# Kernel tuning notes

Measured on AMD Instinct MI355X. Metric: run time of the kernel, lower is better.

The kernel has to match this reference:

```python
import jax, jax.numpy as jnp
import numpy as np

LSTM_DIMS = 1024
T = 4096
D = 1024  # per-direction input width; must equal LSTM_DIMS (see original w shape)
CELL_CLIP = 3.0   # tf.raw_ops.BlockLSTM default
FORGET_BIAS = 1.0  # tf.raw_ops.BlockLSTM default


def setup_inputs() -> dict:
    key = jax.random.key(0)
    k1, k2, k3 = jax.random.split(key, 3)
    res_for_1 = jax.random.normal(k1, (1, T, D), dtype=jnp.float32)
    res_back_1 = jax.random.normal(k2, (1, T, D), dtype=jnp.float32)
    # GlorotUniform for w: shape [D + 2*H, 4*H]
    fan_in, fan_out = D + 2 * LSTM_DIMS, 4 * LSTM_DIMS
    limit = np.sqrt(6.0 / (fan_in + fan_out)).astype(np.float32)
    w = jax.random.uniform(k3, (fan_in, fan_out), dtype=jnp.float32,
                           minval=-limit, maxval=limit)
    return {"res_for_1": res_for_1, "res_back_1": res_back_1, "w": w}


def _bilstm(res_for_1, res_back_1, w):
    H = w.shape[1] // 4
    x_dim = 2 * res_for_1.shape[-1]
    # concatenate_lstm: vec[i] = concat(for[i], back[T-1-i]) -> [T, 2D]
    vec_for = jnp.concatenate([res_for_1[0], res_back_1[0][::-1]], axis=-1)
    vec_back = vec_for[::-1]
    xs = jnp.stack([vec_for, vec_back])            # [2, T, 2D]
    w_x, w_h = w[:x_dim], w[x_dim:]                # [2D,4H], [H,4H]
    # precompute input projection as one big GEMM (bias is zeros)
    zx = jnp.einsum('dtf,fg->dtg', xs, w_x)        # [2, T, 4H]

    def step(carry, zx_t):
        c, h = carry
        z = zx_t + h @ w_h                         # [4H]
        zi, zc, zf, zo = jnp.split(z, 4)           # BlockLSTM icfo order
        i = jax.nn.sigmoid(zi)
        ci = jnp.tanh(zc)
        f = jax.nn.sigmoid(zf + FORGET_BIAS)
        cs = jnp.clip(f * c + i * ci, -CELL_CLIP, CELL_CLIP)
        o = jax.nn.sigmoid(zo)
        h = o * jnp.tanh(cs)
        return (cs, h), h

    init = (jnp.zeros((H,), zx.dtype), jnp.zeros((H,), zx.dtype))

    def run(zx_dir):
        _, hs = jax.lax.scan(step, init, zx_dir)
        return hs                                  # [T, H]

    hs = jax.vmap(run)(zx)                         # [2, T, H]
    return hs[0], hs[1]                            # res_for_2, res_back_2


def reference(res_for_1, res_back_1, w):
    return _bilstm(res_for_1, res_back_1, w)
```

## Files before the change

kernel.cpp:

```cpp
#include <hip/hip_runtime.h>

#define T_STEPS 4096
#define HDIM 1024

typedef __bf16 bf16x8 __attribute__((ext_vector_type(8)));
typedef float f32x4 __attribute__((ext_vector_type(4)));
typedef _Float16 half2_t __attribute__((ext_vector_type(2)));

__device__ __forceinline__ unsigned short f2bf(float x) {
  unsigned u = __builtin_bit_cast(unsigned, x);
  u += 0x7fffu + ((u >> 16) & 1u);
  return (unsigned short)(u >> 16);
}
__device__ __forceinline__ float bf2f(unsigned short b) {
  unsigned u = ((unsigned)b) << 16;
  return __builtin_bit_cast(float, u);
}

__global__ __launch_bounds__(256) void build_xs(
    const float* __restrict__ rf, const float* __restrict__ rb,
    unsigned short* __restrict__ xs) {
  int idx = blockIdx.x * 256 + threadIdx.x;
  int e = idx * 4;
  int f = e & 2047;
  int td = e >> 11;
  int t = td & 4095;
  int d = td >> 12;
  bool lower = f < 1024;
  int f2 = f & 1023;
  int trow;
  if (d == 0) trow = lower ? t : (4095 - t);
  else        trow = lower ? (4095 - t) : t;
  const float* src = (lower ? rf : rb) + trow * 1024 + f2;
  float4 v = *(const float4*)src;
  ushort4 o = make_ushort4(f2bf(v.x), f2bf(v.y), f2bf(v.z), f2bf(v.w));
  *(ushort4*)(xs + e) = o;
}

__global__ __launch_bounds__(256) void transpose_wx(
    const float* __restrict__ w, unsigned short* __restrict__ wxT) {
  __shared__ float tile[64][65];
  int bid = blockIdx.x;
  int bf_ = bid / 64;
  int bg = bid % 64;
  int f0 = bf_ * 64, g0 = bg * 64;
  int tid = threadIdx.x;
#pragma unroll
  for (int s = 0; s < 16; ++s) {
    int idx = s * 256 + tid;
    int fl = idx >> 6, gl = idx & 63;
    tile[fl][gl] = w[(size_t)(f0 + fl) * 4096 + g0 + gl];
  }
  __syncthreads();
#pragma unroll
  for (int s = 0; s < 16; ++s) {
    int idx = s * 256 + tid;
    int gl = idx >> 6, fl = idx & 63;
    wxT[(size_t)(g0 + gl) * 2048 + f0 + fl] = f2bf(tile[fl][gl]);
  }
}

__global__ __launch_bounds__(256) void gemm_zx(
    const unsigned short* __restrict__ xs, const unsigned short* __restrict__ wxT,
    unsigned short* __restrict__ zxo) {
  __shared__ uint4 lds[1024];
  char* ldsb = (char*)lds;
  int bid = blockIdx.x;
  int by = bid >> 5;
  int bx = bid & 31;
  int tid = threadIdx.x, lane = tid & 63, wid = tid >> 6;
  int wr = wid >> 1, wc = wid & 1;
  const int arow0 = by * 128, bcol0 = bx * 128;

  f32x4 acc[4][4] = {};

  for (int kt = 0; kt < 64; ++kt) {
    int k0 = kt * 32;
#pragma unroll
    for (int s = 0; s < 2; ++s) {
      int c = tid + 256 * s;
      int L = c * 16;
      int P = L ^ (((L >> 6) & 7) << 4);
      int row = c >> 2, ko = (c & 3) * 8;
      uint4 av = *(const uint4*)(xs  + (size_t)(arow0 + row) * 2048 + k0 + ko);
      uint4 bv = *(const uint4*)(wxT + (size_t)(bcol0 + row) * 2048 + k0 + ko);
      *(uint4*)(ldsb + P) = av;
      *(uint4*)(ldsb + 8192 + P) = bv;
    }
    __syncthreads();

    bf16x8 afr[4], bfr[4];
#pragma unroll
    for (int i = 0; i < 4; ++i) {
      int arow = wr * 64 + i * 16 + (lane & 15);
      int L = arow * 64 + (lane >> 4) * 16;
      int P = L ^ ((arow & 7) << 4);
      afr[i] = *(bf16x8*)(ldsb + P);
      int brow = wc * 64 + i * 16 + (lane & 15);
      int L2 = brow * 64 + (lane >> 4) * 16;
      int P2 = L2 ^ ((brow & 7) << 4);
      bfr[i] = *(bf16x8*)(ldsb + 8192 + P2);
    }
#pragma unroll
    for (int mi = 0; mi < 4; ++mi)
#pragma unroll
      for (int ni = 0; ni < 4; ++ni)
        acc[mi][ni] = __builtin_amdgcn_mfma_f32_16x16x32_bf16(
            afr[mi], bfr[ni], acc[mi][ni], 0, 0, 0);
    __syncthreads();
  }

#pragma unroll
  for (int mi = 0; mi < 4; ++mi)
#pragma unroll
    for (int ni = 0; ni < 4; ++ni)
#pragma unroll
      for (int r = 0; r < 4; ++r) {
        int rrow = arow0 + wr * 64 + mi * 16 + (lane >> 4) * 4 + r;
        int col  = bcol0 + wc * 64 + ni * 16 + (lane & 15);
        zxo[(size_t)rrow * 4096 + col] = f2bf(acc[mi][ni][r]);
      }
}

__global__ __launch_bounds__(256) void pack_whp(
    const float* __restrict__ w, unsigned* __restrict__ whp) {
  int idx = blockIdx.x * 256 + threadIdx.x;
  int gc = idx & 4095;
  int k2 = idx >> 12;
  float w0 = w[(size_t)(2048 + 2 * k2) * 4096 + gc];
  float w1 = w[(size_t)(2048 + 2 * k2 + 1) * 4096 + gc];
  unsigned short a = __builtin_bit_cast(unsigned short, (_Float16)w0);
  unsigned short b = __builtin_bit_cast(unsigned short, (_Float16)w1);
  whp[idx] = ((unsigned)b << 16) | (unsigned)a;
}

__global__ __launch_bounds__(256) void clear_hcom(uint4* __restrict__ p) {
  p[(size_t)blockIdx.x * 256 + threadIdx.x] = uint4{0, 0, 0, 0};
}

__device__ __forceinline__ float sigm(float x) {
  return 1.0f / (1.0f + __expf(-x));
}
__device__ __forceinline__ float tanh_fast(float x) {
  float e = __expf(-2.0f * x);
  return (1.0f - e) / (1.0f + e);
}

__global__ __launch_bounds__(1024, 4) void lstm_rec(
    const unsigned short* __restrict__ zx,
    const unsigned* __restrict__ whp,
    unsigned* __restrict__ hcom) {
  __shared__ unsigned short hstg[16][64];
  __shared__ float part[2][16][64];

  int bid = blockIdx.x;
  int dir = bid >> 6;
  int bslot = bid & 63;
  int jbase = bslot << 4;
  int tid = threadIdx.x;
  int wave = tid >> 6;
  int lane = tid & 63;
  int jj = lane & 15, g = lane >> 4;
  int gcol = (g << 10) + jbase + jj;

  unsigned wpk[32];
  {
    const unsigned* wp = whp + (size_t)(wave * 32) * 4096 + gcol;
#pragma unroll
    for (int i = 0; i < 32; ++i) wpk[i] = wp[(size_t)i * 4096];
#pragma unroll
    for (int i = 0; i < 32; ++i)
      asm volatile("v_mov_b32 %0, %0" : "+v"(wpk[i]));
  }

  float c_reg = 0.0f;
  const unsigned short* zrow = zx + (size_t)dir * T_STEPS * 4096;
  unsigned* hcd = hcom + (size_t)dir * T_STEPS * HDIM;
  const unsigned* hp_slice = hcd + wave * 64 + lane;

  for (int t = 0; t < T_STEPS; ++t) {
    float zxv = 0.0f;
    if (wave == 15) zxv = bf2f(zrow[(size_t)t * 4096 + gcol]);

    unsigned short hbits = 0;
    if (t > 0) {
      const unsigned* hp = hp_slice + (size_t)(t - 1) * HDIM;
      unsigned want = (unsigned)t << 16;
      unsigned v;
      do {
        v = __hip_atomic_load(hp, __ATOMIC_RELAXED, __HIP_MEMORY_SCOPE_AGENT);
      } while (v < want);
      hbits = (unsigned short)v;
    }
    hstg[wave][lane] = hbits;
    asm volatile("s_waitcnt lgkmcnt(0)" ::: "memory");

    const uint4* h4p = (const uint4*)(&hstg[wave][0]);
    float ac0 = 0.f, ac1 = 0.f, ac2 = 0.f, ac3 = 0.f;
#pragma unroll
    for (int i = 0; i < 8; ++i) {
      uint4 hv = h4p[i];
      ac0 = __builtin_amdgcn_fdot2(__builtin_bit_cast(half2_t, wpk[4 * i + 0]),
                                   __builtin_bit_cast(half2_t, hv.x), ac0, false);
      ac1 = __builtin_amdgcn_fdot2(__builtin_bit_cast(half2_t, wpk[4 * i + 1]),
                                   __builtin_bit_cast(half2_t, hv.y), ac1, false);
      ac2 = __builtin_amdgcn_fdot2(__builtin_bit_cast(half2_t, wpk[4 * i + 2]),
                                   __builtin_bit_cast(half2_t, hv.z), ac2, false);
      ac3 = __builtin_amdgcn_fdot2(__builtin_bit_cast(half2_t, wpk[4 * i + 3]),
                                   __builtin_bit_cast(half2_t, hv.w), ac3, false);
    }
    float acc = (ac0 + ac1) + (ac2 + ac3);
    if (wave == 15) acc += zxv;
    part[t & 1][wave][lane] = acc;
    __syncthreads();

    if (wave == 0) {
      float z = 0.f;
#pragma unroll
      for (int q = 0; q < 16; ++q) z += part[t & 1][q][lane];
      float gz = (g == 2) ? z + 1.0f : z;
      float nl = (g == 1) ? tanh_fast(z) : sigm(gz);
      float iv = __shfl(nl, jj, 64);
      float cv = __shfl(nl, 16 + jj, 64);
      float fv = __shfl(nl, 32 + jj, 64);
      float ov = __shfl(nl, 48 + jj, 64);
      if (lane < 16) {
        float cs = fmaf(fv, c_reg, iv * cv);
        cs = fminf(3.0f, fmaxf(-3.0f, cs));
        c_reg = cs;
        float h = ov * tanh_fast(cs);
        unsigned short hb = __builtin_bit_cast(unsigned short, (_Float16)h);
        unsigned pk = ((unsigned)(t + 1) << 16) | (unsigned)hb;
        __hip_atomic_store(&hcd[(size_t)t * HDIM + jbase + lane], pk,
                           __ATOMIC_RELAXED, __HIP_MEMORY_SCOPE_AGENT);
      }
    }
  }
}

__global__ __launch_bounds__(256) void unpack_out(
    const unsigned* __restrict__ hcom, float* __restrict__ out) {
  int i = blockIdx.x * 256 + threadIdx.x;
  uint4 v = ((const uint4*)hcom)[i];
  float4 o;
  o.x = (float)__builtin_bit_cast(_Float16, (unsigned short)v.x);
  o.y = (float)__builtin_bit_cast(_Float16, (unsigned short)v.y);
  o.z = (float)__builtin_bit_cast(_Float16, (unsigned short)v.z);
  o.w = (float)__builtin_bit_cast(_Float16, (unsigned short)v.w);
  ((float4*)out)[i] = o;
}

extern "C" void kernel_launch(void* const* d_in, const int* in_sizes, int n_in,
                              void* d_out, int out_size, void* d_ws, size_t ws_size,
                              hipStream_t stream) {
  const float* rf = (const float*)d_in[0];
  const float* rb = (const float*)d_in[1];
  const float* w  = (const float*)d_in[2];
  float* out = (float*)d_out;

  char* ws = (char*)d_ws;
  unsigned short* zx  = (unsigned short*)ws;
  unsigned short* xs  = (unsigned short*)(ws + (64u << 20));
  unsigned*      hcom = (unsigned*)(ws + (64u << 20));
  unsigned short* wxT = (unsigned short*)(ws + (96u << 20));
  unsigned*      whp  = (unsigned*)(ws + (96u << 20));

  build_xs<<<16384, 256, 0, stream>>>(rf, rb, xs);
  transpose_wx<<<2048, 256, 0, stream>>>(w, wxT);
  gemm_zx<<<2048, 256, 0, stream>>>(xs, wxT, zx);
  pack_whp<<<8192, 256, 0, stream>>>(w, whp);
  clear_hcom<<<8192, 256, 0, stream>>>((uint4*)hcom);
  lstm_rec<<<128, 1024, 0, stream>>>(zx, whp, hcom);
  unpack_out<<<8192, 256, 0, stream>>>(hcom, out);
}
```

Measured before the change: 6.348 ms.

## Exchange hidden state through replicated ring mailboxes and prefetch next zx

Blocks no longer publish h through the full T×H history buffer. They now write it into an 8-slot ring mailbox that is replicated 8 ways (indexed by bid&7), so each block polls a nearby replica and the polling traffic, which was aimed at one cache line per step, is spread out. The final history is written separately with plain stores by wave 1. The zx value for the next step is now prefetched right after the spin-wait, and the large clear_hcom kernel is replaced by a small memset of the mailbox. Risks: the ring depth of 8 is only safe if no block gets more than 8 steps ahead of the others, and the wider writer path adds extra stores on every step.

```diff
diff --git a/kernel.cpp b/kernel.cpp
--- a/kernel.cpp
+++ b/kernel.cpp
@@ -134,10 +134,6 @@
   whp[idx] = ((unsigned)b << 16) | (unsigned)a;
 }
 
-__global__ __launch_bounds__(256) void clear_hcom(uint4* __restrict__ p) {
-  p[(size_t)blockIdx.x * 256 + threadIdx.x] = uint4{0, 0, 0, 0};
-}
-
 __device__ __forceinline__ float sigm(float x) {
   return 1.0f / (1.0f + __expf(-x));
 }
@@ -149,7 +145,8 @@
 __global__ __launch_bounds__(1024, 4) void lstm_rec(
     const unsigned short* __restrict__ zx,
     const unsigned* __restrict__ whp,
-    unsigned* __restrict__ hcom) {
+    unsigned* __restrict__ hcom,
+    unsigned* __restrict__ mbox) {
   __shared__ unsigned short hstg[16][64];
   __shared__ float part[2][16][64];
 
@@ -176,15 +173,15 @@
   float c_reg = 0.0f;
   const unsigned short* zrow = zx + (size_t)dir * T_STEPS * 4096;
   unsigned* hcd = hcom + (size_t)dir * T_STEPS * HDIM;
-  const unsigned* hp_slice = hcd + wave * 64 + lane;
+  const unsigned* mb_r = mbox + (((size_t)(bid & 7) * 2 + dir) * 8) * 1024;
+
+  float zx_cur = 0.0f;
+  if (wave == 15) zx_cur = bf2f(zrow[gcol]);
 
   for (int t = 0; t < T_STEPS; ++t) {
-    float zxv = 0.0f;
-    if (wave == 15) zxv = bf2f(zrow[(size_t)t * 4096 + gcol]);
-
     unsigned short hbits = 0;
     if (t > 0) {
-      const unsigned* hp = hp_slice + (size_t)(t - 1) * HDIM;
+      const unsigned* hp = mb_r + (size_t)((t - 1) & 7) * 1024 + wave * 64 + lane;
       unsigned want = (unsigned)t << 16;
       unsigned v;
       do {
@@ -192,6 +189,12 @@
       } while (v < want);
       hbits = (unsigned short)v;
     }
+    asm volatile("" ::: "memory");
+
+    float zx_nxt = 0.0f;
+    if (wave == 15 && t + 1 < T_STEPS)
+      zx_nxt = bf2f(zrow[(size_t)(t + 1) * 4096 + gcol]);
+
     hstg[wave][lane] = hbits;
     asm volatile("s_waitcnt lgkmcnt(0)" ::: "memory");
 
@@ -210,11 +213,12 @@
                                    __builtin_bit_cast(half2_t, hv.w), ac3, false);
     }
     float acc = (ac0 + ac1) + (ac2 + ac3);
-    if (wave == 15) acc += zxv;
+    if (wave == 15) acc += zx_cur;
     part[t & 1][wave][lane] = acc;
+    zx_cur = zx_nxt;
     __syncthreads();
 
-    if (wave == 0) {
+    if (wave <= 1) {
       float z = 0.f;
 #pragma unroll
       for (int q = 0; q < 16; ++q) z += part[t & 1][q][lane];
@@ -224,15 +228,21 @@
       float cv = __shfl(nl, 16 + jj, 64);
       float fv = __shfl(nl, 32 + jj, 64);
       float ov = __shfl(nl, 48 + jj, 64);
-      if (lane < 16) {
-        float cs = fmaf(fv, c_reg, iv * cv);
-        cs = fminf(3.0f, fmaxf(-3.0f, cs));
-        c_reg = cs;
-        float h = ov * tanh_fast(cs);
-        unsigned short hb = __builtin_bit_cast(unsigned short, (_Float16)h);
-        unsigned pk = ((unsigned)(t + 1) << 16) | (unsigned)hb;
-        __hip_atomic_store(&hcd[(size_t)t * HDIM + jbase + lane], pk,
+      float cs = fmaf(fv, c_reg, iv * cv);
+      cs = fminf(3.0f, fmaxf(-3.0f, cs));
+      c_reg = cs;
+      float h = ov * tanh_fast(cs);
+      unsigned short hb = __builtin_bit_cast(unsigned short, (_Float16)h);
+      unsigned pk = ((unsigned)(t + 1) << 16) | (unsigned)hb;
+      if (wave == 0) {
+        int c = lane >> 4;
+        size_t slot = (size_t)(t & 7) * 1024 + jbase + jj;
+        __hip_atomic_store(&mbox[(((size_t)c * 2 + dir) * 8) * 1024 + slot], pk,
                            __ATOMIC_RELAXED, __HIP_MEMORY_SCOPE_AGENT);
+        __hip_atomic_store(&mbox[(((size_t)(c + 4) * 2 + dir) * 8) * 1024 + slot], pk,
+                           __ATOMIC_RELAXED, __HIP_MEMORY_SCOPE_AGENT);
+      } else if (lane < 16) {
+        hcd[(size_t)t * HDIM + jbase + lane] = pk;
       }
     }
   }
@@ -264,12 +274,15 @@
   unsigned*      hcom = (unsigned*)(ws + (64u << 20));
   unsigned short* wxT = (unsigned short*)(ws + (96u << 20));
   unsigned*      whp  = (unsigned*)(ws + (96u << 20));
+  unsigned*      mbox = (unsigned*)(ws + (104u << 20));
+
+  const size_t mbox_bytes = 8ull * 2 * 8 * 1024 * 4;
 
   build_xs<<<16384, 256, 0, stream>>>(rf, rb, xs);
   transpose_wx<<<2048, 256, 0, stream>>>(w, wxT);
   gemm_zx<<<2048, 256, 0, stream>>>(xs, wxT, zx);
   pack_whp<<<8192, 256, 0, stream>>>(w, whp);
-  clear_hcom<<<8192, 256, 0, stream>>>((uint4*)hcom);
-  lstm_rec<<<128, 1024, 0, stream>>>(zx, whp, hcom);
+  hipMemsetAsync(mbox, 0, mbox_bytes, stream);
+  lstm_rec<<<128, 1024, 0, stream>>>(zx, whp, hcom, mbox);
   unpack_out<<<8192, 256, 0, stream>>>(hcom, out);
 }
```

Result: slower. 6.842 ms (+7.8%).

## Halve recurrent blocks, give each block 32 hidden units, prefetch next zx

Applied to the files above, without the earlier changes.

The recurrent kernel now runs 64 blocks, each owning 32 hidden units, instead of 128 blocks owning 16. Each thread holds two sets of packed recurrent weights and produces two gate columns. The gate shuffle is simplified to xor-32 exchanges, and the next step's zx value is loaded ahead of time so that load overlaps the spin-wait. Fewer blocks means fewer participants in the per-step cross-block handshake and less polling traffic. The cost is twice the register weight storage per thread and more dot-product work per block on the critical path.

```diff
diff --git a/kernel.cpp b/kernel.cpp
--- a/kernel.cpp
+++ b/kernel.cpp
@@ -151,26 +151,28 @@
     const unsigned* __restrict__ whp,
     unsigned* __restrict__ hcom) {
   __shared__ unsigned short hstg[16][64];
-  __shared__ float part[2][16][64];
+  __shared__ float part[2][16][128];
 
   int bid = blockIdx.x;
-  int dir = bid >> 6;
-  int bslot = bid & 63;
-  int jbase = bslot << 4;
+  int dir = bid >> 5;
+  int bslot = bid & 31;
+  int jbase = bslot << 5;
   int tid = threadIdx.x;
   int wave = tid >> 6;
   int lane = tid & 63;
-  int jj = lane & 15, g = lane >> 4;
-  int gcol = (g << 10) + jbase + jj;
-
-  unsigned wpk[32];
+  int jj = lane & 31;
+  int g0 = lane >> 5;
+  int gcol0 = (g0 << 10) + jbase + jj;
+  int gcol1 = gcol0 + 2048;
+
+  unsigned wpk0[32], wpk1[32];
   {
-    const unsigned* wp = whp + (size_t)(wave * 32) * 4096 + gcol;
-#pragma unroll
-    for (int i = 0; i < 32; ++i) wpk[i] = wp[(size_t)i * 4096];
-#pragma unroll
-    for (int i = 0; i < 32; ++i)
-      asm volatile("v_mov_b32 %0, %0" : "+v"(wpk[i]));
+    const unsigned* wp = whp + (size_t)(wave * 32) * 4096 + gcol0;
+#pragma unroll
+    for (int i = 0; i < 32; ++i) {
+      wpk0[i] = wp[(size_t)i * 4096];
+      wpk1[i] = wp[(size_t)i * 4096 + 2048];
+    }
   }
 
   float c_reg = 0.0f;
@@ -178,10 +180,13 @@
   unsigned* hcd = hcom + (size_t)dir * T_STEPS * HDIM;
   const unsigned* hp_slice = hcd + wave * 64 + lane;
 
+  float zx0 = 0.0f, zx1 = 0.0f;
+  if (wave == 15) {
+    zx0 = bf2f(zrow[gcol0]);
+    zx1 = bf2f(zrow[gcol1]);
+  }
+
   for (int t = 0; t < T_STEPS; ++t) {
-    float zxv = 0.0f;
-    if (wave == 15) zxv = bf2f(zrow[(size_t)t * 4096 + gcol]);
-
     unsigned short hbits = 0;
     if (t > 0) {
       const unsigned* hp = hp_slice + (size_t)(t - 1) * HDIM;
@@ -192,40 +197,57 @@
       } while (v < want);
       hbits = (unsigned short)v;
     }
+    asm volatile("" ::: "memory");
+
+    float zx0n = 0.0f, zx1n = 0.0f;
+    if (wave == 15 && t + 1 < T_STEPS) {
+      zx0n = bf2f(zrow[(size_t)(t + 1) * 4096 + gcol0]);
+      zx1n = bf2f(zrow[(size_t)(t + 1) * 4096 + gcol1]);
+    }
+
     hstg[wave][lane] = hbits;
     asm volatile("s_waitcnt lgkmcnt(0)" ::: "memory");
 
     const uint4* h4p = (const uint4*)(&hstg[wave][0]);
-    float ac0 = 0.f, ac1 = 0.f, ac2 = 0.f, ac3 = 0.f;
+    float a0 = 0.f, a1 = 0.f, b0 = 0.f, b1 = 0.f;
 #pragma unroll
     for (int i = 0; i < 8; ++i) {
       uint4 hv = h4p[i];
-      ac0 = __builtin_amdgcn_fdot2(__builtin_bit_cast(half2_t, wpk[4 * i + 0]),
-                                   __builtin_bit_cast(half2_t, hv.x), ac0, false);
-      ac1 = __builtin_amdgcn_fdot2(__builtin_bit_cast(half2_t, wpk[4 * i + 1]),
-                                   __builtin_bit_cast(half2_t, hv.y), ac1, false);
-      ac2 = __builtin_amdgcn_fdot2(__builtin_bit_cast(half2_t, wpk[4 * i + 2]),
-                                   __builtin_bit_cast(half2_t, hv.z), ac2, false);
-      ac3 = __builtin_amdgcn_fdot2(__builtin_bit_cast(half2_t, wpk[4 * i + 3]),
-                                   __builtin_bit_cast(half2_t, hv.w), ac3, false);
-    }
-    float acc = (ac0 + ac1) + (ac2 + ac3);
-    if (wave == 15) acc += zxv;
-    part[t & 1][wave][lane] = acc;
+      half2_t hx = __builtin_bit_cast(half2_t, hv.x);
+      half2_t hy = __builtin_bit_cast(half2_t, hv.y);
+      half2_t hz = __builtin_bit_cast(half2_t, hv.z);
+      half2_t hw = __builtin_bit_cast(half2_t, hv.w);
+      a0 = __builtin_amdgcn_fdot2(__builtin_bit_cast(half2_t, wpk0[4 * i + 0]), hx, a0, false);
+      a1 = __builtin_amdgcn_fdot2(__builtin_bit_cast(half2_t, wpk0[4 * i + 1]), hy, a1, false);
+      a0 = __builtin_amdgcn_fdot2(__builtin_bit_cast(half2_t, wpk0[4 * i + 2]), hz, a0, false);
+      a1 = __builtin_amdgcn_fdot2(__builtin_bit_cast(half2_t, wpk0[4 * i + 3]), hw, a1, false);
+      b0 = __builtin_amdgcn_fdot2(__builtin_bit_cast(half2_t, wpk1[4 * i + 0]), hx, b0, false);
+      b1 = __builtin_amdgcn_fdot2(__builtin_bit_cast(half2_t, wpk1[4 * i + 1]), hy, b1, false);
+      b0 = __builtin_amdgcn_fdot2(__builtin_bit_cast(half2_t, wpk1[4 * i + 2]), hz, b0, false);
+      b1 = __builtin_amdgcn_fdot2(__builtin_bit_cast(half2_t, wpk1[4 * i + 3]), hw, b1, false);
+    }
+    float acc0 = a0 + a1;
+    float acc1 = b0 + b1;
+    if (wave == 15) { acc0 += zx0; acc1 += zx1; }
+    part[t & 1][wave][lane] = acc0;
+    part[t & 1][wave][lane + 64] = acc1;
+    zx0 = zx0n; zx1 = zx1n;
     __syncthreads();
 
     if (wave == 0) {
-      float z = 0.f;
-#pragma unroll
-      for (int q = 0; q < 16; ++q) z += part[t & 1][q][lane];
-      float gz = (g == 2) ? z + 1.0f : z;
-      float nl = (g == 1) ? tanh_fast(z) : sigm(gz);
-      float iv = __shfl(nl, jj, 64);
-      float cv = __shfl(nl, 16 + jj, 64);
-      float fv = __shfl(nl, 32 + jj, 64);
-      float ov = __shfl(nl, 48 + jj, 64);
-      if (lane < 16) {
-        float cs = fmaf(fv, c_reg, iv * cv);
+      float z0 = 0.f, z1 = 0.f;
+#pragma unroll
+      for (int q = 0; q < 16; ++q) {
+        z0 += part[t & 1][q][lane];
+        z1 += part[t & 1][q][lane + 64];
+      }
+      bool lo = lane < 32;
+      float nl0 = lo ? sigm(z0) : tanh_fast(z0);
+      float nl1 = lo ? sigm(z1 + 1.0f) : sigm(z1);
+      float cv = __shfl_xor(nl0, 32, 64);
+      float ov = __shfl_xor(nl1, 32, 64);
+      if (lo) {
+        float cs = fmaf(nl1, c_reg, nl0 * cv);
         cs = fminf(3.0f, fmaxf(-3.0f, cs));
         c_reg = cs;
         float h = ov * tanh_fast(cs);
@@ -270,6 +292,6 @@
   gemm_zx<<<2048, 256, 0, stream>>>(xs, wxT, zx);
   pack_whp<<<8192, 256, 0, stream>>>(w, whp);
   clear_hcom<<<8192, 256, 0, stream>>>((uint4*)hcom);
-  lstm_rec<<<128, 1024, 0, stream>>>(zx, whp, hcom);
+  lstm_rec<<<64, 1024, 0, stream>>>(zx, whp, hcom);
   unpack_out<<<8192, 256, 0, stream>>>(hcom, out);
 }
```

Result: slower. 7.551 ms (+18.9%).
